# Performance work log

Measured on AMD Instinct MI355X. Metric: run time of the kernel, lower is better.

Reference implementation:

```python
import jax, jax.numpy as jnp
import numpy as np

# Static config matching init_kwargs / input_specs
K = 12      # window size (ks=[12])
S = 4       # stride
D = 48      # spatial grid side; n = D*D = 2304
N = D * D
BS = 8


def _window_indices(d, k, s):
    """Flat token indices for each sliding k x k window over a d x d grid.
    Returns int32 array [num_windows, k*k]."""
    starts = np.arange(0, d - k + 1, s, dtype=np.int64)
    gir, gic = np.meshgrid(starts, starts, indexing='ij')
    rel_a, rel_b = np.meshgrid(np.arange(k, dtype=np.int64), np.arange(k, dtype=np.int64), indexing='ij')
    rel = (rel_a * d + rel_b).ravel()
    idx = (gir.ravel() * d + gic.ravel())[:, None] + rel[None, :]
    return jnp.asarray(idx, dtype=jnp.int32)


def setup_inputs() -> dict:
    key = jax.random.key(0)
    x = jax.random.normal(key, (BS, N, N), dtype=jnp.float32)
    return {"x": x}


def reference(x):
    # Fused row+col submatrix extraction: out[b, w, i, j] = x[b, idx[w, i], idx[w, j]]
    # Shape: [bs, num_windows, k*k, k*k]. Avoids materializing the torch
    # intermediate sub_rows of shape [bs, num_windows, k*k, n].
    idx = _window_indices(D, K, S)                 # [num_windows, k*k]
    return x[:, idx[:, :, None], idx[:, None, :]]  # [bs, nw, k*k, k*k]
```

## Files before the change

### kernel.cpp

```cpp
#include <hip/hip_runtime.h>


#ifndef __align__
#define __align__(x) __attribute__((aligned(x)))
#endif

namespace {
constexpr int NTOK = 2304;
constexpr int NW   = 100;
constexpr int KK   = 144;
constexpr int QPR  = 36;
constexpr int TOTAL_F4 = 8 * NW * KK * QPR;
}

__global__ __launch_bounds__(256) void submanifold_gather(
    const float* __restrict__ x, float4* __restrict__ out) {
    int t = blockIdx.x * 256 + threadIdx.x;

    int q   = t % QPR;
    int rid = t / QPR;
    int i   = rid % KK;
    int bw  = rid / KK;
    int w   = bw % NW;
    int b   = bw / NW;

    int wr = w / 10;
    int wc = w - wr * 10;
    int base = 192 * wr + 4 * wc;

    int ai = i / 12;
    int bi = i - ai * 12;
    int r  = base + 48 * ai + bi;

    int aj  = q / 3;
    int bj4 = (q - aj * 3) * 4;
    int c   = base + 48 * aj + bj4;

    const float4* src = reinterpret_cast<const float4*>(
        x + (size_t)b * NTOK * NTOK + (size_t)r * NTOK + c);
    out[t] = *src;
}

extern "C" void kernel_launch(void* const* d_in, const int* in_sizes, int n_in,
                              void* d_out, int out_size, void* d_ws, size_t ws_size,
                              hipStream_t stream) {
    const float* x = (const float*)d_in[0];
    float4* out = (float4*)d_out;
    const int blocks = TOTAL_F4 / 256;
    submanifold_gather<<<blocks, 256, 0, stream>>>(x, out);
}
```

Before: 231.1 us.

## Stage shared row bands in LDS and emit all windows of a window-row

Each block loads a 48x288 band of the input into swizzled LDS once, then writes the outputs for all ten windows in that window row from LDS. This removes redundant global gathers of overlapping window rows and columns. In exchange it adds a block barrier and about 56KB of LDS per block, which limits occupancy. Load and store phases do not overlap.

```diff
diff --git a/kernel.cpp b/kernel.cpp
--- a/kernel.cpp
+++ b/kernel.cpp
@@ -1,44 +1,62 @@
 #include <hip/hip_runtime.h>
 
 
-#ifndef __align__
-#define __align__(x) __attribute__((aligned(x)))
-#endif
-
 namespace {
-constexpr int NTOK = 2304;
+constexpr int N    = 2304;
 constexpr int NW   = 100;
 constexpr int KK   = 144;
-constexpr int QPR  = 36;
-constexpr int TOTAL_F4 = 8 * NW * KK * QPR;
+constexpr int ROWS = 48;
+constexpr int COLS = 288;
+constexpr int LDSC = 292;
+constexpr int LOAD_F4 = ROWS * (COLS / 4);
+constexpr int OUT_F4  = 10 * 12 * 18;
 }
 
-__global__ __launch_bounds__(256) void submanifold_gather(
+__device__ __forceinline__ int sw(int col) {
+    return col ^ (((col >> 5) & 7) << 2);
+}
+
+__global__ __launch_bounds__(256, 2) void submanifold_band(
     const float* __restrict__ x, float4* __restrict__ out) {
-    int t = blockIdx.x * 256 + threadIdx.x;
+    __shared__ float xs[ROWS][LDSC];
 
-    int q   = t % QPR;
-    int rid = t / QPR;
-    int i   = rid % KK;
-    int bw  = rid / KK;
-    int w   = bw % NW;
-    int b   = bw / NW;
+    int blk = blockIdx.x;
+    int jh  = blk & 1;
+    int t   = blk >> 1;
+    int ai  = t % 12;
+    int bw  = t / 12;
+    int wr  = bw % 10;
+    int b   = bw / 10;
 
-    int wr = w / 10;
-    int wc = w - wr * 10;
-    int base = 192 * wr + 4 * wc;
+    int r0 = 192 * wr + 48 * ai;
+    int c0 = 192 * wr + 288 * jh;
 
-    int ai = i / 12;
-    int bi = i - ai * 12;
-    int r  = base + 48 * ai + bi;
+    const float* xb = x + (size_t)b * N * N;
 
-    int aj  = q / 3;
-    int bj4 = (q - aj * 3) * 4;
-    int c   = base + 48 * aj + bj4;
+    for (int f = threadIdx.x; f < LOAD_F4; f += 256) {
+        int row = f / (COLS / 4);
+        int c4  = f - row * (COLS / 4);
+        float4 v = *reinterpret_cast<const float4*>(
+            xb + (size_t)(r0 + row) * N + c0 + 4 * c4);
+        *reinterpret_cast<float4*>(&xs[row][sw(4 * c4)]) = v;
+    }
+    __syncthreads();
 
-    const float4* src = reinterpret_cast<const float4*>(
-        x + (size_t)b * NTOK * NTOK + (size_t)r * NTOK + c);
-    out[t] = *src;
+    size_t outbase = ((size_t)(b * NW + wr * 10) * KK + 12 * ai) * (KK / 4) + 18 * jh;
+    for (int v = threadIdx.x; v < OUT_F4; v += 256) {
+        int q  = v % 18;
+        int p  = v / 18;
+        int bi = p % 12;
+        int wc = p / 12;
+        int ap  = q / 3;
+        int bj4 = (q - ap * 3) * 4;
+
+        int lrow = 4 * wc + bi;
+        int lcol = 4 * wc + 48 * ap + bj4;
+        float4 val = *reinterpret_cast<const float4*>(&xs[lrow][sw(lcol)]);
+
+        out[outbase + (size_t)wc * (KK * KK / 4) + (size_t)bi * (KK / 4) + q] = val;
+    }
 }
 
 extern "C" void kernel_launch(void* const* d_in, const int* in_sizes, int n_in,
@@ -46,6 +64,6 @@
                               hipStream_t stream) {
     const float* x = (const float*)d_in[0];
     float4* out = (float4*)d_out;
-    const int blocks = TOTAL_F4 / 256;
-    submanifold_gather<<<blocks, 256, 0, stream>>>(x, out);
+    const int blocks = 8 * 10 * 12 * 2;
+    submanifold_band<<<blocks, 256, 0, stream>>>(x, out);
 }
```

Result: slower. 258.4 us (+11.8%).
